# Performance work log

Measured on AMD Instinct MI355X. Metric: run time of the kernel, lower is better.

The kernel has to match this reference:

```python
import jax, jax.numpy as jnp
import numpy as np

B, N, M = 16, 4096, 4096

def setup_inputs() -> dict:
    key = jax.random.key(0)
    k1, k2, k3 = jax.random.split(key, 3)
    src_points = jax.random.normal(k1, (B, N, 3), dtype=jnp.float32)
    tgt_points = jax.random.normal(k2, (B, M, 3), dtype=jnp.float32)
    weights = jax.random.uniform(k3, (B,), dtype=jnp.float32)
    return {"src_points": src_points, "tgt_points": tgt_points, "weights": weights}

def reference(src_points, tgt_points, weights):
    # Pairwise squared distances per batch: [B, N, M]
    # ||s - t||^2 = ||s||^2 + ||t||^2 - 2 s.t  (single dense intermediate)
    s2 = jnp.sum(src_points * src_points, axis=-1)  # [B, N]
    t2 = jnp.sum(tgt_points * tgt_points, axis=-1)  # [B, M]
    cross = jnp.einsum('bnd,bmd->bnm', src_points, tgt_points)  # [B, N, M]
    d2 = s2[:, :, None] + t2[:, None, :] - 2.0 * cross          # [B, N, M]
    d2 = jnp.maximum(d2, 0.0)  # numerical guard
    # Bidirectional chamfer: mean of nearest-neighbor squared distances
    d_src_to_tgt = jnp.mean(jnp.min(d2, axis=2), axis=1)  # [B]
    d_tgt_to_src = jnp.mean(jnp.min(d2, axis=1), axis=1)  # [B]
    distances = d_src_to_tgt + d_tgt_to_src               # [B]
    distances = distances * weights
    return jnp.mean(distances)  # reduction='mean'
```

## Files before the change

### kernel.cpp

```cpp
#include <hip/hip_runtime.h>

#define BQ 16
#define NP 4096
#define MP 4096

constexpr int TPB = 256;
constexpr int SRC_PER_THREAD = 4;
constexpr int NCHUNK = TPB * SRC_PER_THREAD;
constexpr int MSPLIT = 8;
constexpr int MSLICE = MP / MSPLIT;
constexpr int TILE = 256;

__global__ void chamfer_init_kernel(unsigned int* __restrict__ minbuf, int n,
                                    float* __restrict__ out) {
    int i = blockIdx.x * blockDim.x + threadIdx.x;
    if (i < n) minbuf[i] = 0x7F800000u;
    if (i == 0) out[0] = 0.0f;
}

__global__ __launch_bounds__(TPB) void chamfer_dir_kernel(
    const float* __restrict__ srcp,
    const float* __restrict__ tgtp,
    unsigned int* __restrict__ minbuf
) {
    const int bz  = blockIdx.z;
    const int dir = (bz >= BQ) ? 1 : 0;
    const int b   = dir ? (bz - BQ) : bz;

    const float* S = dir ? (tgtp + (size_t)b * MP * 3) : (srcp + (size_t)b * NP * 3);
    const float* T = dir ? (srcp + (size_t)b * NP * 3) : (tgtp + (size_t)b * MP * 3);
    unsigned int* outmin = minbuf + ((size_t)dir * BQ + b) * NP;

    __shared__ float4 tile[TILE];

    const int nbase = blockIdx.x * NCHUNK + threadIdx.x;
    float sx[SRC_PER_THREAD], sy[SRC_PER_THREAD], sz[SRC_PER_THREAD];
#pragma unroll
    for (int k = 0; k < SRC_PER_THREAD; ++k) {
        const float* p = S + (size_t)(nbase + k * TPB) * 3;
        sx[k] = p[0];
        sy[k] = p[1];
        sz[k] = p[2];
    }

    float mn[SRC_PER_THREAD];
#pragma unroll
    for (int k = 0; k < SRC_PER_THREAD; ++k) mn[k] = __int_as_float(0x7F800000);

    const int mbase = blockIdx.y * MSLICE;
    for (int m0 = 0; m0 < MSLICE; m0 += TILE) {
        {
            const float* p = T + (size_t)(mbase + m0 + threadIdx.x) * 3;
            float tx = p[0], ty = p[1], tz = p[2];
            float t2 = fmaf(tx, tx, fmaf(ty, ty, tz * tz));
            tile[threadIdx.x] = make_float4(-2.0f * tx, -2.0f * ty, -2.0f * tz, t2);
        }
        __syncthreads();

#pragma unroll 4
        for (int j = 0; j < TILE; ++j) {
            float4 t = tile[j];
#pragma unroll
            for (int k = 0; k < SRC_PER_THREAD; ++k) {
                float v = fmaf(sx[k], t.x, fmaf(sy[k], t.y, fmaf(sz[k], t.z, t.w)));
                mn[k] = fminf(mn[k], v);
            }
        }
        __syncthreads();
    }

#pragma unroll
    for (int k = 0; k < SRC_PER_THREAD; ++k) {
        float s2 = fmaf(sx[k], sx[k], fmaf(sy[k], sy[k], sz[k] * sz[k]));
        float d  = fmaxf(mn[k] + s2, 0.0f);
        atomicMin(&outmin[nbase + k * TPB], __float_as_uint(d));
    }
}

__global__ __launch_bounds__(TPB) void chamfer_reduce_kernel(
    const float* __restrict__ minbuf,
    const float* __restrict__ weights,
    float* __restrict__ out) {
    const int b = blockIdx.x;
    const float* m0 = minbuf + (size_t)b * NP;
    const float* m1 = minbuf + ((size_t)BQ + b) * NP;

    float s = 0.0f;
    for (int i = threadIdx.x; i < NP; i += TPB) s += m0[i] + m1[i];

#pragma unroll
    for (int off = 32; off > 0; off >>= 1) s += __shfl_down(s, off, 64);

    __shared__ float red[TPB / 64];
    if ((threadIdx.x & 63) == 0) red[threadIdx.x >> 6] = s;
    __syncthreads();
    if (threadIdx.x == 0) {
        float tot = 0.0f;
#pragma unroll
        for (int w = 0; w < TPB / 64; ++w) tot += red[w];
        float val = weights[b] * (tot / (float)NP);
        atomicAdd(out, val / (float)BQ);
    }
}

extern "C" void kernel_launch(void* const* d_in, const int* in_sizes, int n_in,
                              void* d_out, int out_size, void* d_ws, size_t ws_size,
                              hipStream_t stream) {
    const float* src = (const float*)d_in[0];
    const float* tgt = (const float*)d_in[1];
    const float* wts = (const float*)d_in[2];
    float* out = (float*)d_out;

    unsigned int* minbuf = (unsigned int*)d_ws;
    const int minElems = 2 * BQ * NP;

    chamfer_init_kernel<<<(minElems + TPB - 1) / TPB, TPB, 0, stream>>>(
        minbuf, minElems, out);

    dim3 grid(NP / NCHUNK, MSPLIT, 2 * BQ);
    chamfer_dir_kernel<<<grid, TPB, 0, stream>>>(src, tgt, minbuf);

    chamfer_reduce_kernel<<<BQ, TPB, 0, stream>>>((const float*)minbuf, wts, out);
}
```

Measured before the change: 106.5 us.

## Raise per-thread sources, split targets finer into single-tile slices, widen reduce

Doubles sources per thread to 8 and doubles the target split to 16. Each block's target slice is now exactly one 256-point tile, so the tile loop and its two barriers per iteration collapse into one load and one sync. The inner loop handles two targets per step, fusing their mins. The reduce kernel now uses one block per direction and batch, 32 blocks instead of 16. More registers per thread and more atomicMin traffic into the min buffer are the costs.

```diff
diff --git a/kernel.cpp b/kernel.cpp
--- a/kernel.cpp
+++ b/kernel.cpp
@@ -5,9 +5,9 @@
 #define MP 4096
 
 constexpr int TPB = 256;
-constexpr int SRC_PER_THREAD = 4;
+constexpr int SRC_PER_THREAD = 8;
 constexpr int NCHUNK = TPB * SRC_PER_THREAD;
-constexpr int MSPLIT = 8;
+constexpr int MSPLIT = 16;
 constexpr int MSLICE = MP / MSPLIT;
 constexpr int TILE = 256;
 
@@ -33,6 +33,14 @@
 
     __shared__ float4 tile[TILE];
 
+    {
+        const int m = blockIdx.y * MSLICE + threadIdx.x;
+        const float* p = T + (size_t)m * 3;
+        float tx = p[0], ty = p[1], tz = p[2];
+        float t2 = fmaf(tx, tx, fmaf(ty, ty, tz * tz));
+        tile[threadIdx.x] = make_float4(-2.0f * tx, -2.0f * ty, -2.0f * tz, t2);
+    }
+
     const int nbase = blockIdx.x * NCHUNK + threadIdx.x;
     float sx[SRC_PER_THREAD], sy[SRC_PER_THREAD], sz[SRC_PER_THREAD];
 #pragma unroll
@@ -47,26 +55,18 @@
 #pragma unroll
     for (int k = 0; k < SRC_PER_THREAD; ++k) mn[k] = __int_as_float(0x7F800000);
 
-    const int mbase = blockIdx.y * MSLICE;
-    for (int m0 = 0; m0 < MSLICE; m0 += TILE) {
-        {
-            const float* p = T + (size_t)(mbase + m0 + threadIdx.x) * 3;
-            float tx = p[0], ty = p[1], tz = p[2];
-            float t2 = fmaf(tx, tx, fmaf(ty, ty, tz * tz));
-            tile[threadIdx.x] = make_float4(-2.0f * tx, -2.0f * ty, -2.0f * tz, t2);
+    __syncthreads();
+
+#pragma unroll 2
+    for (int j = 0; j < TILE; j += 2) {
+        float4 ta = tile[j];
+        float4 tb = tile[j + 1];
+#pragma unroll
+        for (int k = 0; k < SRC_PER_THREAD; ++k) {
+            float v1 = fmaf(sx[k], ta.x, fmaf(sy[k], ta.y, fmaf(sz[k], ta.z, ta.w)));
+            float v2 = fmaf(sx[k], tb.x, fmaf(sy[k], tb.y, fmaf(sz[k], tb.z, tb.w)));
+            mn[k] = fminf(mn[k], fminf(v1, v2));
         }
-        __syncthreads();
-
-#pragma unroll 4
-        for (int j = 0; j < TILE; ++j) {
-            float4 t = tile[j];
-#pragma unroll
-            for (int k = 0; k < SRC_PER_THREAD; ++k) {
-                float v = fmaf(sx[k], t.x, fmaf(sy[k], t.y, fmaf(sz[k], t.z, t.w)));
-                mn[k] = fminf(mn[k], v);
-            }
-        }
-        __syncthreads();
     }
 
 #pragma unroll
@@ -81,12 +81,12 @@
     const float* __restrict__ minbuf,
     const float* __restrict__ weights,
     float* __restrict__ out) {
-    const int b = blockIdx.x;
-    const float* m0 = minbuf + (size_t)b * NP;
-    const float* m1 = minbuf + ((size_t)BQ + b) * NP;
+    const int idx = blockIdx.x;
+    const int b = idx & (BQ - 1);
+    const float* m0 = minbuf + (size_t)idx * NP;
 
     float s = 0.0f;
-    for (int i = threadIdx.x; i < NP; i += TPB) s += m0[i] + m1[i];
+    for (int i = threadIdx.x; i < NP; i += TPB) s += m0[i];
 
 #pragma unroll
     for (int off = 32; off > 0; off >>= 1) s += __shfl_down(s, off, 64);
@@ -98,8 +98,7 @@
         float tot = 0.0f;
 #pragma unroll
         for (int w = 0; w < TPB / 64; ++w) tot += red[w];
-        float val = weights[b] * (tot / (float)NP);
-        atomicAdd(out, val / (float)BQ);
+        atomicAdd(out, weights[b] * tot * (1.0f / ((float)NP * (float)BQ)));
     }
 }
 
@@ -120,5 +119,5 @@
     dim3 grid(NP / NCHUNK, MSPLIT, 2 * BQ);
     chamfer_dir_kernel<<<grid, TPB, 0, stream>>>(src, tgt, minbuf);
 
-    chamfer_reduce_kernel<<<BQ, TPB, 0, stream>>>((const float*)minbuf, wts, out);
+    chamfer_reduce_kernel<<<2 * BQ, TPB, 0, stream>>>((const float*)minbuf, wts, out);
 }
```

Result: no change. 105.3 us (-1.1%).
